# Performance work log

Hardware: AMD Instinct MI355X
Metric: run time of the kernel (lower is better)

## Reference

```python
import jax, jax.numpy as jnp
import numpy as np

U, N, E, D = 200000, 50000, 1600000, 64


def setup_inputs() -> dict:
    key = jax.random.key(0)
    ks = jax.random.split(key, 8)
    nodes = jax.random.randint(ks[0], (N,), 0, U)
    neigh_idx = jax.random.randint(ks[1], (E,), 0, U)
    seg_ids = jnp.sort(jax.random.randint(ks[2], (E,), 0, N))
    u2e = jax.random.normal(ks[3], (U, D), dtype=jnp.float32) * 0.1
    W1 = jax.random.normal(ks[4], (2 * D, D), dtype=jnp.float32) * 0.1
    b1 = jnp.zeros((D,), dtype=jnp.float32)
    W2 = jax.random.normal(ks[5], (D, D), dtype=jnp.float32) * 0.1
    b2 = jnp.zeros((D,), dtype=jnp.float32)
    w3 = jax.random.normal(ks[6], (D, 1), dtype=jnp.float32) * 0.1
    b3 = jnp.zeros((1,), dtype=jnp.float32)
    return {"nodes": nodes, "neigh_idx": neigh_idx, "seg_ids": seg_ids,
            "u2e": u2e, "W1": W1, "b1": b1, "W2": W2, "b2": b2,
            "w3": w3, "b3": b3}


def reference(nodes, neigh_idx, seg_ids, u2e, W1, b1, W2, b2, w3, b3):
    # Per-node self representation  [N, D]
    u_rep = u2e[nodes]
    # Ragged neighbor gather flattened to edge list
    e_u = u2e[neigh_idx]                      # [E, D]
    u_edge = u_rep[seg_ids]                   # [E, D] node rep broadcast to its edges
    # Attention MLP (GraphRec-style), eval mode (no dropout)
    x = jnp.concatenate([e_u, u_edge], axis=1)            # [E, 2D]
    x = jax.nn.relu(x @ W1 + b1)
    x = jax.nn.relu(x @ W2 + b2)
    logits = (x @ w3 + b3)[:, 0]                           # [E]
    # Segment softmax over each node's neighbor set
    seg_max = jax.ops.segment_max(logits, seg_ids, num_segments=N)
    ex = jnp.exp(logits - seg_max[seg_ids])
    denom = jax.ops.segment_sum(ex, seg_ids, num_segments=N)
    att = ex / denom[seg_ids]                              # [E]
    # Attention-weighted neighbor aggregation: e_u^T @ att per node
    agg = jax.ops.segment_sum(att[:, None] * e_u, seg_ids, num_segments=N)  # [N, D]
    # Nodes with zero neighbors fall back to their own embedding
    counts = jax.ops.segment_sum(jnp.ones((E,), dtype=jnp.float32), seg_ids, num_segments=N)
    out = jnp.where(counts[:, None] > 0, agg, u_rep)
    return out
```

## Files before the change

### kernel.cpp

```cpp
#include <hip/hip_runtime.h>
#include <math.h>

#define D 64

typedef __fp16 fp16x2 __attribute__((ext_vector_type(2)));
typedef _Float16 half8 __attribute__((ext_vector_type(8)));
typedef _Float16 half4v __attribute__((ext_vector_type(4)));
typedef __attribute__((ext_vector_type(4))) float f32x4;

union h8pun { half8 v; fp16x2 h2[4]; };

__global__ __launch_bounds__(256) void k_prep(const float* __restrict__ W1,
                                              const float* __restrict__ W2,
                                              float* __restrict__ W1at,
                                              float* __restrict__ W1bt,
                                              float* __restrict__ W2pt,
                                              const int* __restrict__ seg_ids,
                                              int* __restrict__ start, int E, int N) {
    int i = blockIdx.x * 256 + threadIdx.x;
    if (i < 3 * D * D) {
        int mat = i / (D * D), j = i % (D * D);
        if (mat == 0) {
            int r = j >> 6, c = j & 63;
            W1at[c * D + r] = W1[r * D + c];
        } else if (mat == 1) {
            int r = j >> 6, c = j & 63;
            W1bt[c * D + r] = W1[(D + r) * D + c];
        } else {
            int n = j >> 6, pos = j & 63;
            int k = (pos >> 2) + 16 * (pos & 3);
            W2pt[n * D + pos] = W2[k * D + n];
        }
    }
    if (i <= N) {
        int lo = 0, hi = E;
        while (lo < hi) {
            int mid = (lo + hi) >> 1;
            if (seg_ids[mid] < i) lo = mid + 1; else hi = mid;
        }
        start[i] = lo;
    }
}

__global__ __launch_bounds__(256) void k_proj_both(const float* __restrict__ u2e,
                                                   const int* __restrict__ nodes,
                                                   const float* __restrict__ W1at,
                                                   const float* __restrict__ W1bt,
                                                   const float* __restrict__ b1,
                                                   _Float16* __restrict__ q,
                                                   _Float16* __restrict__ u2e_h,
                                                   _Float16* __restrict__ p,
                                                   int U, int N, int wavesU, int wavesN) {
    int lane = threadIdx.x & 63;
    int m = lane & 15, quad = lane >> 4;
    int wave = (blockIdx.x * blockDim.x + threadIdx.x) >> 6;

    const float* Wt;
    const int* idx;
    const float* bias;
    _Float16* outp;
    _Float16* copyp;
    int R, w0, wstride;
    if (wave < wavesU) {
        Wt = W1at; idx = nullptr; bias = nullptr; outp = q; copyp = u2e_h;
        R = U; w0 = wave; wstride = wavesU;
    } else {
        Wt = W1bt; idx = nodes; bias = b1; outp = p; copyp = nullptr;
        R = N; w0 = wave - wavesU; wstride = wavesN;
    }

    half8 Bf[2][4];
    float bv[4];
#pragma unroll
    for (int t = 0; t < 4; ++t) {
        int n = m + 16 * t;
        bv[t] = bias ? bias[n] : 0.0f;
#pragma unroll
        for (int kh = 0; kh < 2; ++kh) {
            const float* col = Wt + n * D + kh * 32 + quad * 8;
#pragma unroll
            for (int j = 0; j < 8; ++j) Bf[kh][t][j] = (_Float16)col[j];
        }
    }

    int ngroups = (R + 15) / 16;
    for (int g = w0; g < ngroups; g += wstride) {
        int r_ = g * 16 + m;
        int rs = r_ < R ? r_ : R - 1;
        int src = idx ? idx[rs] : rs;
        const float4* arow = (const float4*)(u2e + (size_t)src * D);
        float4 x0 = arow[quad * 2], x1 = arow[quad * 2 + 1];
        float4 y0 = arow[8 + quad * 2], y1 = arow[8 + quad * 2 + 1];
        h8pun A0, A1;
        A0.h2[0] = __builtin_amdgcn_cvt_pkrtz(x0.x, x0.y);
        A0.h2[1] = __builtin_amdgcn_cvt_pkrtz(x0.z, x0.w);
        A0.h2[2] = __builtin_amdgcn_cvt_pkrtz(x1.x, x1.y);
        A0.h2[3] = __builtin_amdgcn_cvt_pkrtz(x1.z, x1.w);
        A1.h2[0] = __builtin_amdgcn_cvt_pkrtz(y0.x, y0.y);
        A1.h2[1] = __builtin_amdgcn_cvt_pkrtz(y0.z, y0.w);
        A1.h2[2] = __builtin_amdgcn_cvt_pkrtz(y1.x, y1.y);
        A1.h2[3] = __builtin_amdgcn_cvt_pkrtz(y1.z, y1.w);
        if (copyp && r_ < R) {
            *(half8*)(copyp + (size_t)r_ * D + quad * 8) = A0.v;
            *(half8*)(copyp + (size_t)r_ * D + 32 + quad * 8) = A1.v;
        }
        f32x4 C[4];
#pragma unroll
        for (int t = 0; t < 4; ++t) C[t] = (f32x4){bv[t], bv[t], bv[t], bv[t]};
#pragma unroll
        for (int t = 0; t < 4; ++t) {
            C[t] = __builtin_amdgcn_mfma_f32_16x16x32_f16(A0.v, Bf[0][t], C[t], 0, 0, 0);
            C[t] = __builtin_amdgcn_mfma_f32_16x16x32_f16(A1.v, Bf[1][t], C[t], 0, 0, 0);
        }
#pragma unroll
        for (int r = 0; r < 4; ++r) {
            int row = g * 16 + quad * 4 + r;
            if (row < R) {
                half4v hv = {(_Float16)C[0][r], (_Float16)C[1][r],
                             (_Float16)C[2][r], (_Float16)C[3][r]};
                *(half4v*)(outp + (size_t)row * D + m * 4) = hv;
            }
        }
    }
}

__global__ __launch_bounds__(256) void k_edge_logits_mfma(const int* __restrict__ neigh_idx,
                                                          const int* __restrict__ seg_ids,
                                                          const _Float16* __restrict__ q,
                                                          const _Float16* __restrict__ p,
                                                          const float* __restrict__ W2pt,
                                                          const float* __restrict__ b2,
                                                          const float* __restrict__ w3,
                                                          const float* __restrict__ b3,
                                                          float* __restrict__ logits, int E) {
    int lane = threadIdx.x & 63;
    int m = lane & 15, quad = lane >> 4;

    half8 Bf[2][4];
    float b2v[4], w3v[4];
#pragma unroll
    for (int t = 0; t < 4; ++t) {
        int n = m + 16 * t;
        b2v[t] = b2[n];
        w3v[t] = w3[n];
#pragma unroll
        for (int kh = 0; kh < 2; ++kh) {
            const float* col = W2pt + n * D + kh * 32 + quad * 8;
#pragma unroll
            for (int j = 0; j < 8; ++j) Bf[kh][t][j] = (_Float16)col[j];
        }
    }
    float b3v = b3[0];
    const half8 hz = {0, 0, 0, 0, 0, 0, 0, 0};

    int ngroups = (E + 31) / 32;
    int wave = (blockIdx.x * blockDim.x + threadIdx.x) >> 6;
    int nwaves = (gridDim.x * blockDim.x) >> 6;
    for (int g = wave; g < ngroups; g += nwaves) {
        int ea = g * 32 + m, eb = ea + 16;
        int eas = ea < E ? ea : E - 1;
        int ebs = eb < E ? eb : E - 1;
        int nbra = neigh_idx[eas], sega = seg_ids[eas];
        int nbrb = neigh_idx[ebs], segb = seg_ids[ebs];
        const half8* qra = (const half8*)(q + (size_t)nbra * D);
        const half8* pra = (const half8*)(p + (size_t)sega * D);
        const half8* qrb = (const half8*)(q + (size_t)nbrb * D);
        const half8* prb = (const half8*)(p + (size_t)segb * D);
        half8 qa0 = qra[quad], qa1 = qra[quad + 4];
        half8 pa0 = pra[quad], pa1 = pra[quad + 4];
        half8 qb0 = qrb[quad], qb1 = qrb[quad + 4];
        half8 pb0 = prb[quad], pb1 = prb[quad + 4];
        half8 Aa0 = __builtin_elementwise_max(qa0 + pa0, hz);
        half8 Aa1 = __builtin_elementwise_max(qa1 + pa1, hz);
        half8 Ab0 = __builtin_elementwise_max(qb0 + pb0, hz);
        half8 Ab1 = __builtin_elementwise_max(qb1 + pb1, hz);
        f32x4 Ca[4], Cb[4];
#pragma unroll
        for (int t = 0; t < 4; ++t) {
            Ca[t] = (f32x4){b2v[t], b2v[t], b2v[t], b2v[t]};
            Cb[t] = Ca[t];
        }
#pragma unroll
        for (int t = 0; t < 4; ++t) {
            Ca[t] = __builtin_amdgcn_mfma_f32_16x16x32_f16(Aa0, Bf[0][t], Ca[t], 0, 0, 0);
            Ca[t] = __builtin_amdgcn_mfma_f32_16x16x32_f16(Aa1, Bf[1][t], Ca[t], 0, 0, 0);
            Cb[t] = __builtin_amdgcn_mfma_f32_16x16x32_f16(Ab0, Bf[0][t], Cb[t], 0, 0, 0);
            Cb[t] = __builtin_amdgcn_mfma_f32_16x16x32_f16(Ab1, Bf[1][t], Cb[t], 0, 0, 0);
        }
        float pa[4], pb[4];
#pragma unroll
        for (int r = 0; r < 4; ++r) {
            float sa = 0.0f, sb = 0.0f;
#pragma unroll
            for (int t = 0; t < 4; ++t) {
                sa += fmaxf(Ca[t][r], 0.0f) * w3v[t];
                sb += fmaxf(Cb[t][r], 0.0f) * w3v[t];
            }
            pa[r] = sa; pb[r] = sb;
        }
#pragma unroll
        for (int off = 1; off <= 8; off <<= 1) {
#pragma unroll
            for (int r = 0; r < 4; ++r) {
                pa[r] += __shfl_xor(pa[r], off, 64);
                pb[r] += __shfl_xor(pb[r], off, 64);
            }
        }
        if (m == 0) {
            int e0 = g * 32 + quad * 4;
            if (e0 + 3 < E)
                *(float4*)(logits + e0) = make_float4(pa[0] + b3v, pa[1] + b3v, pa[2] + b3v, pa[3] + b3v);
            else
#pragma unroll
                for (int r = 0; r < 4; ++r)
                    if (e0 + r < E) logits[e0 + r] = pa[r] + b3v;
            int e1 = e0 + 16;
            if (e1 + 3 < E)
                *(float4*)(logits + e1) = make_float4(pb[0] + b3v, pb[1] + b3v, pb[2] + b3v, pb[3] + b3v);
            else
#pragma unroll
                for (int r = 0; r < 4; ++r)
                    if (e1 + r < E) logits[e1 + r] = pb[r] + b3v;
        }
    }
}

__global__ __launch_bounds__(256) void k_agg(const int* __restrict__ nodes,
                                             const int* __restrict__ neigh_idx,
                                             const float* __restrict__ u2e,
                                             const _Float16* __restrict__ u2e_h,
                                             const float* __restrict__ logits,
                                             const int* __restrict__ start,
                                             float* __restrict__ out, int N) {
    int n = blockIdx.x * 4 + ((int)threadIdx.x >> 6);
    int lane = threadIdx.x & 63;
    if (n >= N) return;
    int s = start[n];
    int t = start[n + 1];
    if (s == t) {
        int node = nodes[n];
        out[(size_t)n * D + lane] = u2e[(size_t)node * D + lane];
        return;
    }
    float mx = -INFINITY;
    for (int i = s + lane; i < t; i += 64) mx = fmaxf(mx, logits[i]);
#pragma unroll
    for (int off = 32; off >= 1; off >>= 1) mx = fmaxf(mx, __shfl_xor(mx, off, 64));
    float ssum = 0.0f;
    for (int i = s + lane; i < t; i += 64) ssum += __expf(logits[i] - mx);
#pragma unroll
    for (int off = 32; off >= 1; off >>= 1) ssum += __shfl_xor(ssum, off, 64);
    float inv = 1.0f / ssum;

    int grp = lane >> 3, sub = lane & 7;
    float acc[8];
#pragma unroll
    for (int j = 0; j < 8; ++j) acc[j] = 0.0f;
    for (int i = s; i < t; i += 32) {
#pragma unroll
        for (int uu = 0; uu < 4; ++uu) {
            int ii = i + uu * 8 + grp;
            bool v = ii < t;
            int is = v ? ii : s;
            float lg = logits[is];
            int nb = neigh_idx[is];
            half8 r = *(const half8*)(u2e_h + (size_t)nb * D + sub * 8);
            float a = v ? __expf(lg - mx) * inv : 0.0f;
#pragma unroll
            for (int j = 0; j < 8; ++j) acc[j] += a * (float)r[j];
        }
    }
#pragma unroll
    for (int off = 8; off <= 32; off <<= 1) {
#pragma unroll
        for (int j = 0; j < 8; ++j) acc[j] += __shfl_xor(acc[j], off, 64);
    }
    if (grp == 0) {
        float* o = out + (size_t)n * D + sub * 8;
        *(float4*)o = make_float4(acc[0], acc[1], acc[2], acc[3]);
        *(float4*)(o + 4) = make_float4(acc[4], acc[5], acc[6], acc[7]);
    }
}

extern "C" void kernel_launch(void* const* d_in, const int* in_sizes, int n_in,
                              void* d_out, int out_size, void* d_ws, size_t ws_size,
                              hipStream_t stream) {
    const int* nodes = (const int*)d_in[0];
    const int* neigh_idx = (const int*)d_in[1];
    const int* seg_ids = (const int*)d_in[2];
    const float* u2e = (const float*)d_in[3];
    const float* W1 = (const float*)d_in[4];
    const float* b1 = (const float*)d_in[5];
    const float* W2 = (const float*)d_in[6];
    const float* b2 = (const float*)d_in[7];
    const float* w3 = (const float*)d_in[8];
    const float* b3 = (const float*)d_in[9];
    float* out = (float*)d_out;

    int N = in_sizes[0];
    int E = in_sizes[1];
    int U = in_sizes[3] / D;

    char* ws = (char*)d_ws;
    size_t off = 0;
    auto alloc = [&](size_t bytes) {
        void* ptr = ws + off;
        off = (off + bytes + 255) & ~(size_t)255;
        return ptr;
    };
    float* logits = (float*)alloc((size_t)E * 4);
    int* start = (int*)alloc((size_t)(N + 1) * 4);
    float* W1at = (float*)alloc((size_t)D * D * 4);
    float* W1bt = (float*)alloc((size_t)D * D * 4);
    float* W2pt = (float*)alloc((size_t)D * D * 4);
    _Float16* q = (_Float16*)alloc((size_t)U * D * 2);
    _Float16* p = (_Float16*)alloc((size_t)N * D * 2);
    _Float16* u2e_h = (_Float16*)alloc((size_t)U * D * 2);
    (void)ws_size;

    int prep_n = (N + 1) > 3 * D * D ? (N + 1) : 3 * D * D;
    k_prep<<<(prep_n + 255) / 256, 256, 0, stream>>>(W1, W2, W1at, W1bt, W2pt,
                                                     seg_ids, start, E, N);
    const int wavesU = 4096, wavesN = 1024;
    k_proj_both<<<(wavesU + wavesN) / 4, 256, 0, stream>>>(u2e, nodes, W1at, W1bt, b1,
                                                           q, u2e_h, p, U, N, wavesU, wavesN);
    k_edge_logits_mfma<<<2048, 256, 0, stream>>>(neigh_idx, seg_ids, q, p, W2pt,
                                                 b2, w3, b3, logits, E);
    k_agg<<<(N + 3) / 4, 256, 0, stream>>>(nodes, neigh_idx, u2e, u2e_h, logits, start, out, N);
}
```

Measured before the change: 239.4 us.

## Fuse edge-logit MLP and segment softmax aggregation into one online-softmax kernel

Merges the per-edge MLP logits kernel and the per-node aggregation kernel into a single per-node kernel. Each node's wave computes logits for 16 edges at a time with MFMA and applies an online softmax with a running max and rescaled accumulators. This removes the logits buffer write/read, the separate max and sum passes, and one launch. W2 is pre-converted to fp16 in the prep kernel. In exchange, the per-node wave loses work when a node has fewer than 16 edges (about 32 on average here), reloads W2 per wave, and no longer reuses p across edges within a group.

Measured after the change: 286.0 us. +19.5%, slower.

```diff
diff --git a/kernel.cpp b/kernel.cpp
--- a/kernel.cpp
+++ b/kernel.cpp
@@ -14,7 +14,7 @@
                                               const float* __restrict__ W2,
                                               float* __restrict__ W1at,
                                               float* __restrict__ W1bt,
-                                              float* __restrict__ W2pt,
+                                              _Float16* __restrict__ W2h,
                                               const int* __restrict__ seg_ids,
                                               int* __restrict__ start, int E, int N) {
     int i = blockIdx.x * 256 + threadIdx.x;
@@ -29,7 +29,7 @@
         } else {
             int n = j >> 6, pos = j & 63;
             int k = (pos >> 2) + 16 * (pos & 3);
-            W2pt[n * D + pos] = W2[k * D + n];
+            W2h[n * D + pos] = (_Float16)W2[k * D + n];
         }
     }
     if (i <= N) {
@@ -124,114 +124,18 @@
     }
 }
 
-__global__ __launch_bounds__(256) void k_edge_logits_mfma(const int* __restrict__ neigh_idx,
-                                                          const int* __restrict__ seg_ids,
-                                                          const _Float16* __restrict__ q,
-                                                          const _Float16* __restrict__ p,
-                                                          const float* __restrict__ W2pt,
-                                                          const float* __restrict__ b2,
-                                                          const float* __restrict__ w3,
-                                                          const float* __restrict__ b3,
-                                                          float* __restrict__ logits, int E) {
-    int lane = threadIdx.x & 63;
-    int m = lane & 15, quad = lane >> 4;
-
-    half8 Bf[2][4];
-    float b2v[4], w3v[4];
-#pragma unroll
-    for (int t = 0; t < 4; ++t) {
-        int n = m + 16 * t;
-        b2v[t] = b2[n];
-        w3v[t] = w3[n];
-#pragma unroll
-        for (int kh = 0; kh < 2; ++kh) {
-            const float* col = W2pt + n * D + kh * 32 + quad * 8;
-#pragma unroll
-            for (int j = 0; j < 8; ++j) Bf[kh][t][j] = (_Float16)col[j];
-        }
-    }
-    float b3v = b3[0];
-    const half8 hz = {0, 0, 0, 0, 0, 0, 0, 0};
-
-    int ngroups = (E + 31) / 32;
-    int wave = (blockIdx.x * blockDim.x + threadIdx.x) >> 6;
-    int nwaves = (gridDim.x * blockDim.x) >> 6;
-    for (int g = wave; g < ngroups; g += nwaves) {
-        int ea = g * 32 + m, eb = ea + 16;
-        int eas = ea < E ? ea : E - 1;
-        int ebs = eb < E ? eb : E - 1;
-        int nbra = neigh_idx[eas], sega = seg_ids[eas];
-        int nbrb = neigh_idx[ebs], segb = seg_ids[ebs];
-        const half8* qra = (const half8*)(q + (size_t)nbra * D);
-        const half8* pra = (const half8*)(p + (size_t)sega * D);
-        const half8* qrb = (const half8*)(q + (size_t)nbrb * D);
-        const half8* prb = (const half8*)(p + (size_t)segb * D);
-        half8 qa0 = qra[quad], qa1 = qra[quad + 4];
-        half8 pa0 = pra[quad], pa1 = pra[quad + 4];
-        half8 qb0 = qrb[quad], qb1 = qrb[quad + 4];
-        half8 pb0 = prb[quad], pb1 = prb[quad + 4];
-        half8 Aa0 = __builtin_elementwise_max(qa0 + pa0, hz);
-        half8 Aa1 = __builtin_elementwise_max(qa1 + pa1, hz);
-        half8 Ab0 = __builtin_elementwise_max(qb0 + pb0, hz);
-        half8 Ab1 = __builtin_elementwise_max(qb1 + pb1, hz);
-        f32x4 Ca[4], Cb[4];
-#pragma unroll
-        for (int t = 0; t < 4; ++t) {
-            Ca[t] = (f32x4){b2v[t], b2v[t], b2v[t], b2v[t]};
-            Cb[t] = Ca[t];
-        }
-#pragma unroll
-        for (int t = 0; t < 4; ++t) {
-            Ca[t] = __builtin_amdgcn_mfma_f32_16x16x32_f16(Aa0, Bf[0][t], Ca[t], 0, 0, 0);
-            Ca[t] = __builtin_amdgcn_mfma_f32_16x16x32_f16(Aa1, Bf[1][t], Ca[t], 0, 0, 0);
-            Cb[t] = __builtin_amdgcn_mfma_f32_16x16x32_f16(Ab0, Bf[0][t], Cb[t], 0, 0, 0);
-            Cb[t] = __builtin_amdgcn_mfma_f32_16x16x32_f16(Ab1, Bf[1][t], Cb[t], 0, 0, 0);
-        }
-        float pa[4], pb[4];
-#pragma unroll
-        for (int r = 0; r < 4; ++r) {
-            float sa = 0.0f, sb = 0.0f;
-#pragma unroll
-            for (int t = 0; t < 4; ++t) {
-                sa += fmaxf(Ca[t][r], 0.0f) * w3v[t];
-                sb += fmaxf(Cb[t][r], 0.0f) * w3v[t];
-            }
-            pa[r] = sa; pb[r] = sb;
-        }
-#pragma unroll
-        for (int off = 1; off <= 8; off <<= 1) {
-#pragma unroll
-            for (int r = 0; r < 4; ++r) {
-                pa[r] += __shfl_xor(pa[r], off, 64);
-                pb[r] += __shfl_xor(pb[r], off, 64);
-            }
-        }
-        if (m == 0) {
-            int e0 = g * 32 + quad * 4;
-            if (e0 + 3 < E)
-                *(float4*)(logits + e0) = make_float4(pa[0] + b3v, pa[1] + b3v, pa[2] + b3v, pa[3] + b3v);
-            else
-#pragma unroll
-                for (int r = 0; r < 4; ++r)
-                    if (e0 + r < E) logits[e0 + r] = pa[r] + b3v;
-            int e1 = e0 + 16;
-            if (e1 + 3 < E)
-                *(float4*)(logits + e1) = make_float4(pb[0] + b3v, pb[1] + b3v, pb[2] + b3v, pb[3] + b3v);
-            else
-#pragma unroll
-                for (int r = 0; r < 4; ++r)
-                    if (e1 + r < E) logits[e1 + r] = pb[r] + b3v;
-        }
-    }
-}
-
-__global__ __launch_bounds__(256) void k_agg(const int* __restrict__ nodes,
-                                             const int* __restrict__ neigh_idx,
-                                             const float* __restrict__ u2e,
-                                             const _Float16* __restrict__ u2e_h,
-                                             const float* __restrict__ logits,
-                                             const int* __restrict__ start,
-                                             float* __restrict__ out, int N) {
+__global__ __launch_bounds__(256) void k_fused(const int* __restrict__ nodes,
+                                               const int* __restrict__ neigh_idx,
+                                               const float* __restrict__ u2e,
+                                               const _Float16* __restrict__ u2e_h,
+                                               const _Float16* __restrict__ q,
+                                               const _Float16* __restrict__ p,
+                                               const _Float16* __restrict__ W2h,
+                                               const float* __restrict__ b2,
+                                               const float* __restrict__ w3,
+                                               const float* __restrict__ b3,
+                                               const int* __restrict__ start,
+                                               float* __restrict__ out, int N) {
     int n = blockIdx.x * 4 + ((int)threadIdx.x >> 6);
     int lane = threadIdx.x & 63;
     if (n >= N) return;
@@ -242,34 +146,99 @@
         out[(size_t)n * D + lane] = u2e[(size_t)node * D + lane];
         return;
     }
-    float mx = -INFINITY;
-    for (int i = s + lane; i < t; i += 64) mx = fmaxf(mx, logits[i]);
-#pragma unroll
-    for (int off = 32; off >= 1; off >>= 1) mx = fmaxf(mx, __shfl_xor(mx, off, 64));
-    float ssum = 0.0f;
-    for (int i = s + lane; i < t; i += 64) ssum += __expf(logits[i] - mx);
-#pragma unroll
-    for (int off = 32; off >= 1; off >>= 1) ssum += __shfl_xor(ssum, off, 64);
-    float inv = 1.0f / ssum;
+    int m = lane & 15, quad = lane >> 4;
+
+    half8 Bf[2][4];
+    float b2v[4], w3v[4];
+#pragma unroll
+    for (int tt = 0; tt < 4; ++tt) {
+        int nn = m + 16 * tt;
+        b2v[tt] = b2[nn];
+        w3v[tt] = w3[nn];
+        Bf[0][tt] = *(const half8*)(W2h + nn * D + quad * 8);
+        Bf[1][tt] = *(const half8*)(W2h + nn * D + 32 + quad * 8);
+    }
+    float b3v = b3[0];
+    const half8 hz = {0, 0, 0, 0, 0, 0, 0, 0};
+
+    const half8* pr = (const half8*)(p + (size_t)n * D);
+    half8 p0 = pr[quad], p1 = pr[quad + 4];
 
     int grp = lane >> 3, sub = lane & 7;
+    float m_run = -INFINITY, denom = 0.0f;
     float acc[8];
 #pragma unroll
     for (int j = 0; j < 8; ++j) acc[j] = 0.0f;
-    for (int i = s; i < t; i += 32) {
-#pragma unroll
-        for (int uu = 0; uu < 4; ++uu) {
-            int ii = i + uu * 8 + grp;
-            bool v = ii < t;
-            int is = v ? ii : s;
-            float lg = logits[is];
-            int nb = neigh_idx[is];
-            half8 r = *(const half8*)(u2e_h + (size_t)nb * D + sub * 8);
-            float a = v ? __expf(lg - mx) * inv : 0.0f;
-#pragma unroll
-            for (int j = 0; j < 8; ++j) acc[j] += a * (float)r[j];
-        }
-    }
+
+    int cnt = t - s;
+    int nbr = neigh_idx[s + (m < cnt ? m : 0)];
+    for (int b0 = 0; b0 < cnt; b0 += 16) {
+        int nbr_c = nbr;
+        const half8* qr = (const half8*)(q + (size_t)nbr_c * D);
+        half8 q0 = qr[quad], q1 = qr[quad + 4];
+        if (b0 + 16 < cnt) {
+            int nx = b0 + 16 + m;
+            nbr = neigh_idx[s + (nx < cnt ? nx : 0)];
+        }
+        half8 A0 = __builtin_elementwise_max(q0 + p0, hz);
+        half8 A1 = __builtin_elementwise_max(q1 + p1, hz);
+        f32x4 C[4];
+#pragma unroll
+        for (int tt = 0; tt < 4; ++tt) C[tt] = (f32x4){b2v[tt], b2v[tt], b2v[tt], b2v[tt]};
+#pragma unroll
+        for (int tt = 0; tt < 4; ++tt) {
+            C[tt] = __builtin_amdgcn_mfma_f32_16x16x32_f16(A0, Bf[0][tt], C[tt], 0, 0, 0);
+            C[tt] = __builtin_amdgcn_mfma_f32_16x16x32_f16(A1, Bf[1][tt], C[tt], 0, 0, 0);
+        }
+        float pa[4];
+#pragma unroll
+        for (int r = 0; r < 4; ++r) {
+            float sa = 0.0f;
+#pragma unroll
+            for (int tt = 0; tt < 4; ++tt) sa += fmaxf(C[tt][r], 0.0f) * w3v[tt];
+            pa[r] = sa;
+        }
+#pragma unroll
+        for (int off = 1; off <= 8; off <<= 1) {
+#pragma unroll
+            for (int r = 0; r < 4; ++r) pa[r] += __shfl_xor(pa[r], off, 64);
+        }
+#pragma unroll
+        for (int r = 0; r < 4; ++r) {
+            pa[r] += b3v;
+            if (b0 + quad * 4 + r >= cnt) pa[r] = -INFINITY;
+        }
+        float bm = fmaxf(fmaxf(pa[0], pa[1]), fmaxf(pa[2], pa[3]));
+        bm = fmaxf(bm, __shfl_xor(bm, 16, 64));
+        bm = fmaxf(bm, __shfl_xor(bm, 32, 64));
+        float mn = fmaxf(m_run, bm);
+        float scale = __expf(m_run - mn);
+        float sb = __expf(pa[0] - mn) + __expf(pa[1] - mn) +
+                   __expf(pa[2] - mn) + __expf(pa[3] - mn);
+        sb += __shfl_xor(sb, 16, 64);
+        sb += __shfl_xor(sb, 32, 64);
+        denom = denom * scale + sb;
+#pragma unroll
+        for (int j = 0; j < 8; ++j) acc[j] *= scale;
+        m_run = mn;
+#pragma unroll
+        for (int rd = 0; rd < 2; ++rd) {
+            int le = rd * 8 + grp;
+            int src = (le >> 2) << 4;
+            float t0 = __shfl(pa[0], src, 64);
+            float t1 = __shfl(pa[1], src, 64);
+            float t2 = __shfl(pa[2], src, 64);
+            float t3 = __shfl(pa[3], src, 64);
+            int rs = le & 3;
+            float l = rs == 0 ? t0 : rs == 1 ? t1 : rs == 2 ? t2 : t3;
+            int nb = __shfl(nbr_c, le, 64);
+            float w = __expf(l - mn);
+            half8 r8 = *(const half8*)(u2e_h + (size_t)nb * D + sub * 8);
+#pragma unroll
+            for (int j = 0; j < 8; ++j) acc[j] += w * (float)r8[j];
+        }
+    }
+    float inv = 1.0f / denom;
 #pragma unroll
     for (int off = 8; off <= 32; off <<= 1) {
 #pragma unroll
@@ -277,8 +246,8 @@
     }
     if (grp == 0) {
         float* o = out + (size_t)n * D + sub * 8;
-        *(float4*)o = make_float4(acc[0], acc[1], acc[2], acc[3]);
-        *(float4*)(o + 4) = make_float4(acc[4], acc[5], acc[6], acc[7]);
+        *(float4*)o = make_float4(acc[0] * inv, acc[1] * inv, acc[2] * inv, acc[3] * inv);
+        *(float4*)(o + 4) = make_float4(acc[4] * inv, acc[5] * inv, acc[6] * inv, acc[7] * inv);
     }
 }
 
@@ -308,23 +277,21 @@
         off = (off + bytes + 255) & ~(size_t)255;
         return ptr;
     };
-    float* logits = (float*)alloc((size_t)E * 4);
     int* start = (int*)alloc((size_t)(N + 1) * 4);
     float* W1at = (float*)alloc((size_t)D * D * 4);
     float* W1bt = (float*)alloc((size_t)D * D * 4);
-    float* W2pt = (float*)alloc((size_t)D * D * 4);
+    _Float16* W2h = (_Float16*)alloc((size_t)D * D * 2);
     _Float16* q = (_Float16*)alloc((size_t)U * D * 2);
     _Float16* p = (_Float16*)alloc((size_t)N * D * 2);
     _Float16* u2e_h = (_Float16*)alloc((size_t)U * D * 2);
     (void)ws_size;
 
     int prep_n = (N + 1) > 3 * D * D ? (N + 1) : 3 * D * D;
-    k_prep<<<(prep_n + 255) / 256, 256, 0, stream>>>(W1, W2, W1at, W1bt, W2pt,
+    k_prep<<<(prep_n + 255) / 256, 256, 0, stream>>>(W1, W2, W1at, W1bt, W2h,
                                                      seg_ids, start, E, N);
     const int wavesU = 4096, wavesN = 1024;
     k_proj_both<<<(wavesU + wavesN) / 4, 256, 0, stream>>>(u2e, nodes, W1at, W1bt, b1,
                                                            q, u2e_h, p, U, N, wavesU, wavesN);
-    k_edge_logits_mfma<<<2048, 256, 0, stream>>>(neigh_idx, seg_ids, q, p, W2pt,
-                                                 b2, w3, b3, logits, E);
-    k_agg<<<(N + 3) / 4, 256, 0, stream>>>(nodes, neigh_idx, u2e, u2e_h, logits, start, out, N);
-}
+    k_fused<<<(N + 3) / 4, 256, 0, stream>>>(nodes, neigh_idx, u2e, u2e_h, q, p,
+                                             W2h, b2, w3, b3, start, out, N);
+}
```

## Compute softmax numerators in edge kernel and accumulate denominators via segmented atomics

Applied to the files above, without the earlier changes.

The edge kernel now exponentiates logits directly, with no max subtraction, and writes exp values. It also reduces per-segment sums within each wave and atomically adds them into a zeroed denominator array. The aggregation kernel drops its two passes over logits (max and sum) and scales the final accumulator by 1/denom. W2 is pre-converted to fp16 in prep, and the projection grid is enlarged. Skipping the max subtraction relies on logits being small enough that exp does not overflow, and the atomic accumulation makes the float sums non-deterministic.

Result: no change. 236.1 us (-1.4%).

```diff
diff --git a/kernel.cpp b/kernel.cpp
--- a/kernel.cpp
+++ b/kernel.cpp
@@ -14,9 +14,11 @@
                                               const float* __restrict__ W2,
                                               float* __restrict__ W1at,
                                               float* __restrict__ W1bt,
-                                              float* __restrict__ W2pt,
+                                              _Float16* __restrict__ W2h,
                                               const int* __restrict__ seg_ids,
-                                              int* __restrict__ start, int E, int N) {
+                                              int* __restrict__ start,
+                                              float* __restrict__ denom,
+                                              int E, int N) {
     int i = blockIdx.x * 256 + threadIdx.x;
     if (i < 3 * D * D) {
         int mat = i / (D * D), j = i % (D * D);
@@ -29,7 +31,7 @@
         } else {
             int n = j >> 6, pos = j & 63;
             int k = (pos >> 2) + 16 * (pos & 3);
-            W2pt[n * D + pos] = W2[k * D + n];
+            W2h[n * D + pos] = (_Float16)W2[k * D + n];
         }
     }
     if (i <= N) {
@@ -40,6 +42,7 @@
         }
         start[i] = lo;
     }
+    if (i < N) denom[i] = 0.0f;
 }
 
 __global__ __launch_bounds__(256) void k_proj_both(const float* __restrict__ u2e,
@@ -124,15 +127,16 @@
     }
 }
 
-__global__ __launch_bounds__(256) void k_edge_logits_mfma(const int* __restrict__ neigh_idx,
-                                                          const int* __restrict__ seg_ids,
-                                                          const _Float16* __restrict__ q,
-                                                          const _Float16* __restrict__ p,
-                                                          const float* __restrict__ W2pt,
-                                                          const float* __restrict__ b2,
-                                                          const float* __restrict__ w3,
-                                                          const float* __restrict__ b3,
-                                                          float* __restrict__ logits, int E) {
+__global__ __launch_bounds__(256) void k_edge_ex(const int* __restrict__ neigh_idx,
+                                                 const int* __restrict__ seg_ids,
+                                                 const _Float16* __restrict__ q,
+                                                 const _Float16* __restrict__ p,
+                                                 const _Float16* __restrict__ W2h,
+                                                 const float* __restrict__ b2,
+                                                 const float* __restrict__ w3,
+                                                 const float* __restrict__ b3,
+                                                 float* __restrict__ exb,
+                                                 float* __restrict__ denom, int E) {
     int lane = threadIdx.x & 63;
     int m = lane & 15, quad = lane >> 4;
 
@@ -143,12 +147,8 @@
         int n = m + 16 * t;
         b2v[t] = b2[n];
         w3v[t] = w3[n];
-#pragma unroll
-        for (int kh = 0; kh < 2; ++kh) {
-            const float* col = W2pt + n * D + kh * 32 + quad * 8;
-#pragma unroll
-            for (int j = 0; j < 8; ++j) Bf[kh][t][j] = (_Float16)col[j];
-        }
+        Bf[0][t] = *(const half8*)(W2h + n * D + quad * 8);
+        Bf[1][t] = *(const half8*)(W2h + n * D + 32 + quad * 8);
     }
     float b3v = b3[0];
     const half8 hz = {0, 0, 0, 0, 0, 0, 0, 0};
@@ -206,32 +206,63 @@
                 pb[r] += __shfl_xor(pb[r], off, 64);
             }
         }
+#pragma unroll
+        for (int r = 0; r < 4; ++r) {
+            int eea = g * 32 + quad * 4 + r;
+            pa[r] = eea < E ? __expf(pa[r] + b3v) : 0.0f;
+            pb[r] = eea + 16 < E ? __expf(pb[r] + b3v) : 0.0f;
+        }
         if (m == 0) {
             int e0 = g * 32 + quad * 4;
             if (e0 + 3 < E)
-                *(float4*)(logits + e0) = make_float4(pa[0] + b3v, pa[1] + b3v, pa[2] + b3v, pa[3] + b3v);
+                *(float4*)(exb + e0) = make_float4(pa[0], pa[1], pa[2], pa[3]);
             else
 #pragma unroll
                 for (int r = 0; r < 4; ++r)
-                    if (e0 + r < E) logits[e0 + r] = pa[r] + b3v;
+                    if (e0 + r < E) exb[e0 + r] = pa[r];
             int e1 = e0 + 16;
             if (e1 + 3 < E)
-                *(float4*)(logits + e1) = make_float4(pb[0] + b3v, pb[1] + b3v, pb[2] + b3v, pb[3] + b3v);
+                *(float4*)(exb + e1) = make_float4(pb[0], pb[1], pb[2], pb[3]);
             else
 #pragma unroll
                 for (int r = 0; r < 4; ++r)
-                    if (e1 + r < E) logits[e1 + r] = pb[r] + b3v;
-        }
-    }
-}
-
-__global__ __launch_bounds__(256) void k_agg(const int* __restrict__ nodes,
-                                             const int* __restrict__ neigh_idx,
-                                             const float* __restrict__ u2e,
-                                             const _Float16* __restrict__ u2e_h,
-                                             const float* __restrict__ logits,
-                                             const int* __restrict__ start,
-                                             float* __restrict__ out, int N) {
+                    if (e1 + r < E) exb[e1 + r] = pb[r];
+        }
+        int l2 = lane & 31;
+        int srcl = ((l2 & 15) >> 2) << 4;
+        float a0 = __shfl(pa[0], srcl, 64), a1 = __shfl(pa[1], srcl, 64);
+        float a2 = __shfl(pa[2], srcl, 64), a3 = __shfl(pa[3], srcl, 64);
+        float c0 = __shfl(pb[0], srcl, 64), c1 = __shfl(pb[1], srcl, 64);
+        float c2 = __shfl(pb[2], srcl, 64), c3 = __shfl(pb[3], srcl, 64);
+        int r2 = l2 & 3;
+        float exa = r2 == 0 ? a0 : r2 == 1 ? a1 : r2 == 2 ? a2 : a3;
+        float exc = r2 == 0 ? c0 : r2 == 1 ? c1 : r2 == 2 ? c2 : c3;
+        float exl = l2 < 16 ? exa : exc;
+        int sga = __shfl(sega, l2 & 15, 64);
+        int sgb = __shfl(segb, l2 & 15, 64);
+        int sgl = l2 < 16 ? sga : sgb;
+        bool active = (lane < 32) && (g * 32 + l2 < E);
+        while (__any(active)) {
+            int s0 = active ? sgl : 0x7fffffff;
+#pragma unroll
+            for (int off = 1; off <= 32; off <<= 1) s0 = min(s0, __shfl_xor(s0, off, 64));
+            float c = (active && sgl == s0) ? exl : 0.0f;
+#pragma unroll
+            for (int off = 1; off <= 32; off <<= 1) c += __shfl_xor(c, off, 64);
+            if (lane == 0) atomicAdd(&denom[s0], c);
+            if (sgl == s0) active = false;
+        }
+    }
+}
+
+__global__ __launch_bounds__(256) void k_agg_fast(const int* __restrict__ nodes,
+                                                  const int* __restrict__ neigh_idx,
+                                                  const float* __restrict__ u2e,
+                                                  const _Float16* __restrict__ u2e_h,
+                                                  const float* __restrict__ exb,
+                                                  const float* __restrict__ denom,
+                                                  const int* __restrict__ start,
+                                                  float* __restrict__ out, int N) {
     int n = blockIdx.x * 4 + ((int)threadIdx.x >> 6);
     int lane = threadIdx.x & 63;
     if (n >= N) return;
@@ -242,15 +273,7 @@
         out[(size_t)n * D + lane] = u2e[(size_t)node * D + lane];
         return;
     }
-    float mx = -INFINITY;
-    for (int i = s + lane; i < t; i += 64) mx = fmaxf(mx, logits[i]);
-#pragma unroll
-    for (int off = 32; off >= 1; off >>= 1) mx = fmaxf(mx, __shfl_xor(mx, off, 64));
-    float ssum = 0.0f;
-    for (int i = s + lane; i < t; i += 64) ssum += __expf(logits[i] - mx);
-#pragma unroll
-    for (int off = 32; off >= 1; off >>= 1) ssum += __shfl_xor(ssum, off, 64);
-    float inv = 1.0f / ssum;
+    float inv = 1.0f / denom[n];
 
     int grp = lane >> 3, sub = lane & 7;
     float acc[8];
@@ -262,12 +285,12 @@
             int ii = i + uu * 8 + grp;
             bool v = ii < t;
             int is = v ? ii : s;
-            float lg = logits[is];
+            float w = exb[is];
             int nb = neigh_idx[is];
             half8 r = *(const half8*)(u2e_h + (size_t)nb * D + sub * 8);
-            float a = v ? __expf(lg - mx) * inv : 0.0f;
-#pragma unroll
-            for (int j = 0; j < 8; ++j) acc[j] += a * (float)r[j];
+            if (!v) w = 0.0f;
+#pragma unroll
+            for (int j = 0; j < 8; ++j) acc[j] += w * (float)r[j];
         }
     }
 #pragma unroll
@@ -277,8 +300,8 @@
     }
     if (grp == 0) {
         float* o = out + (size_t)n * D + sub * 8;
-        *(float4*)o = make_float4(acc[0], acc[1], acc[2], acc[3]);
-        *(float4*)(o + 4) = make_float4(acc[4], acc[5], acc[6], acc[7]);
+        *(float4*)o = make_float4(acc[0] * inv, acc[1] * inv, acc[2] * inv, acc[3] * inv);
+        *(float4*)(o + 4) = make_float4(acc[4] * inv, acc[5] * inv, acc[6] * inv, acc[7] * inv);
     }
 }
 
@@ -308,23 +331,25 @@
         off = (off + bytes + 255) & ~(size_t)255;
         return ptr;
     };
-    float* logits = (float*)alloc((size_t)E * 4);
+    float* exb = (float*)alloc((size_t)E * 4);
     int* start = (int*)alloc((size_t)(N + 1) * 4);
+    float* denom = (float*)alloc((size_t)N * 4);
     float* W1at = (float*)alloc((size_t)D * D * 4);
     float* W1bt = (float*)alloc((size_t)D * D * 4);
-    float* W2pt = (float*)alloc((size_t)D * D * 4);
+    _Float16* W2h = (_Float16*)alloc((size_t)D * D * 2);
     _Float16* q = (_Float16*)alloc((size_t)U * D * 2);
     _Float16* p = (_Float16*)alloc((size_t)N * D * 2);
     _Float16* u2e_h = (_Float16*)alloc((size_t)U * D * 2);
     (void)ws_size;
 
     int prep_n = (N + 1) > 3 * D * D ? (N + 1) : 3 * D * D;
-    k_prep<<<(prep_n + 255) / 256, 256, 0, stream>>>(W1, W2, W1at, W1bt, W2pt,
-                                                     seg_ids, start, E, N);
-    const int wavesU = 4096, wavesN = 1024;
+    k_prep<<<(prep_n + 255) / 256, 256, 0, stream>>>(W1, W2, W1at, W1bt, W2h,
+                                                     seg_ids, start, denom, E, N);
+    const int wavesU = 6144, wavesN = 2048;
     k_proj_both<<<(wavesU + wavesN) / 4, 256, 0, stream>>>(u2e, nodes, W1at, W1bt, b1,
                                                            q, u2e_h, p, U, N, wavesU, wavesN);
-    k_edge_logits_mfma<<<2048, 256, 0, stream>>>(neigh_idx, seg_ids, q, p, W2pt,
-                                                 b2, w3, b3, logits, E);
-    k_agg<<<(N + 3) / 4, 256, 0, stream>>>(nodes, neigh_idx, u2e, u2e_h, logits, start, out, N);
-}
+    k_edge_ex<<<2048, 256, 0, stream>>>(neigh_idx, seg_ids, q, p, W2h,
+                                        b2, w3, b3, exb, denom, E);
+    k_agg_fast<<<(N + 3) / 4, 256, 0, stream>>>(nodes, neigh_idx, u2e, u2e_h,
+                                                exb, denom, start, out, N);
+}
```
